# Kernel optimization log

Hardware: AMD Instinct MI355X
Metric: run time of the kernel (lower is better)

The kernel has to match this reference:

```python
import jax, jax.numpy as jnp
import numpy as np

SIZE = 32            # resize target from size=(32,32)
CAL_THRESH = 0.3
WIN = 11             # standard SSIM gaussian window
SIGMA = 1.5
C1 = (0.01 * 255.0) ** 2   # data range 255 (patches are raw pixel values)
C2 = (0.03 * 255.0) ** 2


def _gauss_window():
    g = np.exp(-((np.arange(WIN) - WIN // 2) ** 2) / (2.0 * SIGMA ** 2))
    g = g / g.sum()
    return jnp.asarray(np.outer(g, g), jnp.float32)


def _gconv(x, win):
    # depthwise gaussian blur, same padding; x: [N,C,H,W]
    C = x.shape[1]
    k = jnp.tile(win[None, None], (C, 1, 1, 1))
    return jax.lax.conv_general_dilated(
        x, k, (1, 1), 'SAME',
        dimension_numbers=('NCHW', 'OIHW', 'NCHW'), feature_group_count=C)


def _crop_resize(img, box):
    # img: [C,H,W]; box: [x,y,w,h] with (x,y) = top-left (as used by the crop).
    # Equivalent to img[:, int(y):int(y+h), int(x):int(x+w)] then bilinear
    # F.interpolate to (SIZE,SIZE), align_corners=False (edge-clamped).
    C, H, W = img.shape
    x0 = jnp.floor(box[0]); y0 = jnp.floor(box[1])
    w = jnp.floor(box[0] + box[2]) - x0   # int(x+w) - int(x)
    h = jnp.floor(box[1] + box[3]) - y0
    ys = jnp.clip((jnp.arange(SIZE, dtype=jnp.float32) + 0.5) * (h / SIZE) - 0.5,
                  0.0, jnp.maximum(h - 1.0, 0.0))
    xs = jnp.clip((jnp.arange(SIZE, dtype=jnp.float32) + 0.5) * (w / SIZE) - 0.5,
                  0.0, jnp.maximum(w - 1.0, 0.0))
    yf = jnp.floor(ys); xf = jnp.floor(xs)
    wy = (ys - yf)[None, :, None]   # row weights
    wx = (xs - xf)[None, None, :]   # col weights

    def gi(yi, xi):
        yi = jnp.clip(yi, 0, H - 1).astype(jnp.int32)
        xi = jnp.clip(xi, 0, W - 1).astype(jnp.int32)
        return img[:, yi[:, None], xi[None, :]]  # [C,SIZE,SIZE]

    ylo = yf + y0; yhi = jnp.minimum(yf + 1.0, jnp.maximum(h - 1.0, 0.0)) + y0
    xlo = xf + x0; xhi = jnp.minimum(xf + 1.0, jnp.maximum(w - 1.0, 0.0)) + x0
    top = gi(ylo, xlo) * (1.0 - wx) + gi(ylo, xhi) * wx
    bot = gi(yhi, xlo) * (1.0 - wx) + gi(yhi, xhi) * wx
    return top * (1.0 - wy) + bot * wy


def _pairwise_iou(gt, pr):
    # faithful to get_two_box_iou: (x,y) treated as CENTER here (source quirk)
    g = gt[:, :, None, :]; p = pr[:, None, :, :]
    tl = jnp.maximum(g[..., :2] - g[..., 2:] / 2, p[..., :2] - p[..., 2:] / 2)
    br = jnp.minimum(g[..., :2] + g[..., 2:] / 2, p[..., :2] + p[..., 2:] / 2)
    en = jnp.prod((tl < br).astype(gt.dtype), axis=-1)
    area_i = jnp.prod(br - tl, axis=-1) * en
    area_g = jnp.prod(gt[..., 2:], axis=-1)[:, :, None]
    area_p = jnp.prod(pr[..., 2:], axis=-1)[:, None, :]
    return area_i / (area_g + area_p - area_i + 1e-16)  # [B,G,P]


def setup_inputs() -> dict:
    key = jax.random.key(0)
    k1, k2, k3, k4, k5 = jax.random.split(key, 5)
    B, G, P, H, W = 8, 16, 64, 640, 640
    imgs = jax.random.uniform(k1, (B, 3, H, W), jnp.float32) * 255.0
    xy = jax.random.uniform(k2, (B, G, 2), jnp.float32) * (W - 80.0) + 4.0
    wh = jax.random.uniform(k3, (B, G, 2), jnp.float32) * 56.0 + 8.0
    gt_boxes = jnp.concatenate([xy, wh], axis=-1)
    base = jnp.tile(gt_boxes, (1, P // G, 1))  # preds jittered around GTs so IoU>thresh often
    jit_xy = jax.random.uniform(k4, (B, P, 2), jnp.float32, -4.0, 4.0)
    jit_wh = jax.random.uniform(k5, (B, P, 2), jnp.float32, -4.0, 4.0)
    pred_boxes = jnp.concatenate(
        [base[..., :2] + jit_xy, jnp.maximum(base[..., 2:] + jit_wh, 3.0)], axis=-1)
    return {"gt_boxes": gt_boxes, "pred_boxes": pred_boxes, "imgs": imgs}


def reference(gt_boxes, pred_boxes, imgs):
    B, G = gt_boxes.shape[:2]; P = pred_boxes.shape[1]
    crop = jax.vmap(jax.vmap(_crop_resize, in_axes=(None, 0)), in_axes=(0, 0))
    gt_patch = crop(imgs, gt_boxes)     # [B,G,3,S,S]
    pr_patch = crop(imgs, pred_boxes)   # [B,P,3,S,S]

    iou = _pairwise_iou(gt_boxes, pred_boxes)                    # [B,G,P]
    valid = (pred_boxes[..., 2] > 2) & (pred_boxes[..., 3] > 2)  # [B,P]
    mask = ((iou > CAL_THRESH) & valid[:, None, :]).astype(imgs.dtype)

    # surviving pairs -> dense pair grid (masked mean == mean over survivors)
    x = jnp.broadcast_to(pr_patch[:, None], (B, G, P, 3, SIZE, SIZE)).reshape(-1, 3, SIZE, SIZE)
    y = jnp.broadcast_to(gt_patch[:, :, None], (B, G, P, 3, SIZE, SIZE)).reshape(-1, 3, SIZE, SIZE)

    win = _gauss_window()
    mu1 = _gconv(x, win); mu2 = _gconv(y, win)
    mu1_sq = mu1 * mu1; mu2_sq = mu2 * mu2; mu12 = mu1 * mu2
    s1 = _gconv(x * x, win) - mu1_sq
    s2 = _gconv(y * y, win) - mu2_sq
    s12 = _gconv(x * y, win) - mu12
    ssim_map = ((2 * mu12 + C1) * (2 * s12 + C2)) / ((mu1_sq + mu2_sq + C1) * (s1 + s2 + C2))

    loss = jnp.abs(x / 255.0 - y / 255.0) + (1.0 - ssim_map)    # L1 + SSIM loss, [N,3,S,S]
    loss = loss.reshape(B, G, P, 3, SIZE, SIZE)
    m = mask[:, :, :, None, None, None]
    cnt = jnp.sum(mask) * (3 * SIZE * SIZE)
    total = jnp.sum(loss * m)
    return jnp.where(cnt > 0, total / jnp.maximum(cnt, 1.0), 0.0)
```

## Files before the change

kernel.cpp:

```cpp
#include <hip/hip_runtime.h>
#include <math.h>

#define TSIZE 32
#define WIN 11
#define NB 8
#define NG 16
#define NP 64
#define IMH 640
#define IMW 640
#define NBOX 640
#define NPAIR 8192
#define NCOMP (NPAIR/256)
#define K2GRID 1536

#define C1F 6.5025f
#define C2F 58.5225f

struct GaussW { float g[WIN]; };
struct f4 { float v[4]; };

__global__ __launch_bounds__(256) void gen_patches(
    const float* __restrict__ gt_boxes, const float* __restrict__ pred_boxes,
    const float* __restrict__ imgs,
    float* __restrict__ patches, float* __restrict__ mus, float* __restrict__ gsqs,
    int* __restrict__ pair_list, int* __restrict__ pair_cnt, GaussW gw)
{
    const int bid = blockIdx.x;
    const int tid = threadIdx.x;

    if (bid >= NBOX * 3) {
        const int blk = bid - NBOX * 3;
        const int p = blk * 256 + tid;
        const int b  = p >> 10;
        const int gi = (p >> 6) & 15;
        const int pi = p & 63;
        bool mask;
        {
#pragma clang fp contract(off)
            const float* gb = gt_boxes  + ((size_t)b * NG + gi) * 4;
            const float* pb = pred_boxes + ((size_t)b * NP + pi) * 4;
            const float gx = gb[0], gy = gb[1], gw_ = gb[2], gh = gb[3];
            const float px = pb[0], py = pb[1], pw = pb[2], ph = pb[3];
            const float tlx = fmaxf(gx - gw_ / 2.0f, px - pw / 2.0f);
            const float tly = fmaxf(gy - gh / 2.0f, py - ph / 2.0f);
            const float brx = fminf(gx + gw_ / 2.0f, px + pw / 2.0f);
            const float bry = fminf(gy + gh / 2.0f, py + ph / 2.0f);
            const float en = ((tlx < brx) ? 1.0f : 0.0f) * ((tly < bry) ? 1.0f : 0.0f);
            const float ai = ((brx - tlx) * (bry - tly)) * en;
            const float ag = gw_ * gh;
            const float ap = pw * ph;
            const float iou = ai / (ag + ap - ai + 1e-16f);
            mask = (iou > 0.3f) && (pw > 2.0f) && (ph > 2.0f);
        }
        __shared__ int wcnt[4], woff[4];
        const unsigned long long bal = __ballot(mask);
        const int lane = tid & 63, wid = tid >> 6;
        if (lane == 0) wcnt[wid] = __popcll(bal);
        __syncthreads();
        if (tid == 0) {
            int s = 0;
#pragma unroll
            for (int w = 0; w < 4; ++w) { woff[w] = s; s += wcnt[w]; }
            pair_cnt[blk] = s;
        }
        __syncthreads();
        if (mask) {
            const int pre = __popcll(bal & ((1ull << lane) - 1ull));
            pair_list[blk * 256 + woff[wid] + pre] = p;
        }
        return;
    }

    const int box = bid / 3;
    const int c   = bid - box * 3;
    int b;
    const float* boxp;
    if (box < NB * NG) {
        b = box >> 4;
        boxp = gt_boxes + (size_t)box * 4;
    } else {
        const int q = box - NB * NG;
        b = q >> 6;
        boxp = pred_boxes + (size_t)q * 4;
    }
    const float* __restrict__ ic = imgs + ((size_t)b * 3 + c) * (IMH * IMW);
    float* __restrict__ patch_o = patches + ((size_t)box * 3 + c) * 1024;
    float* __restrict__ mu_o    = mus     + ((size_t)box * 3 + c) * 1024;
    float* __restrict__ gsq_o   = gsqs    + ((size_t)box * 3 + c) * 1024;

    __shared__ int   s_ylo[TSIZE], s_yhi[TSIZE], s_xlo[TSIZE], s_xhi[TSIZE];
    __shared__ float s_wy[TSIZE], s_wx[TSIZE];
    __shared__ __align__(16) float smem[4900];
    float* const sp = smem;
    float* const ta = smem + 1024;
    float* const tb = smem + 2048;

    {
#pragma clang fp contract(off)
        const float b0 = boxp[0], b1 = boxp[1], b2 = boxp[2], b3 = boxp[3];
        const float x0 = floorf(b0), y0 = floorf(b1);
        const float w = floorf(b0 + b2) - x0;
        const float h = floorf(b1 + b3) - y0;

        if (tid < TSIZE) {
            const int t = tid;
            const float hm = fmaxf(h - 1.0f, 0.0f);
            const float scale = h / 32.0f;
            float ys = ((float)t + 0.5f) * scale - 0.5f;
            ys = fminf(fmaxf(ys, 0.0f), hm);
            const float yf = floorf(ys);
            s_wy[t] = ys - yf;
            const float ylo = yf + y0;
            const float yhi = fminf(yf + 1.0f, hm) + y0;
            s_ylo[t] = (int)fminf(fmaxf(ylo, 0.0f), (float)(IMH - 1));
            s_yhi[t] = (int)fminf(fmaxf(yhi, 0.0f), (float)(IMH - 1));
        } else if (tid < 2 * TSIZE) {
            const int t = tid - TSIZE;
            const float wm = fmaxf(w - 1.0f, 0.0f);
            const float scale = w / 32.0f;
            float xs = ((float)t + 0.5f) * scale - 0.5f;
            xs = fminf(fmaxf(xs, 0.0f), wm);
            const float xf = floorf(xs);
            s_wx[t] = xs - xf;
            const float xlo = xf + x0;
            const float xhi = fminf(xf + 1.0f, wm) + x0;
            s_xlo[t] = (int)fminf(fmaxf(xlo, 0.0f), (float)(IMW - 1));
            s_xhi[t] = (int)fminf(fmaxf(xhi, 0.0f), (float)(IMW - 1));
        }
    }
    __syncthreads();

    const int ry0 = s_ylo[0], ry1 = s_yhi[31];
    const int rx0 = s_xlo[0], rx1 = s_xhi[31];
    const int RH = ry1 - ry0 + 1;
    const int RW = rx1 - rx0 + 1;
    const int stride = RW | 1;
    {
        const int wid  = tid >> 6;
        const int lane = tid & 63;
        for (int r = wid; r < RH; r += 4) {
            const float* __restrict__ src = ic + (size_t)(ry0 + r) * IMW + rx0;
            float* __restrict__ dst = smem + r * stride;
            for (int cc = lane; cc < RW; cc += 64) dst[cc] = src[cc];
        }
    }
    __syncthreads();

    const int i  = tid >> 3;
    const int j4 = (tid & 7) << 2;
    const int e4 = (i << 5) + j4;

    float vv[4];
    {
        const int yl = s_ylo[i] - ry0, yh = s_yhi[i] - ry0;
        const float wy = s_wy[i];
#pragma unroll
        for (int q = 0; q < 4; ++q) {
#pragma clang fp contract(off)
            const int j = j4 + q;
            const int xl = s_xlo[j] - rx0, xh = s_xhi[j] - rx0;
            const float wx = s_wx[j];
            const float tl = smem[yl * stride + xl], tr = smem[yl * stride + xh];
            const float bl = smem[yh * stride + xl], br = smem[yh * stride + xh];
            const float top = tl * (1.0f - wx) + tr * wx;
            const float bot = bl * (1.0f - wx) + br * wx;
            vv[q] = top * (1.0f - wy) + bot * wy;
        }
    }
    __syncthreads();

    {
        f4 o; o.v[0] = vv[0]; o.v[1] = vv[1]; o.v[2] = vv[2]; o.v[3] = vv[3];
        *(f4*)&sp[e4] = o;
        *(f4*)&patch_o[e4] = o;
    }
    __syncthreads();

    {
        float pv[14];
#pragma unroll
        for (int k = 0; k < 14; ++k) {
            const int jj = j4 - 5 + k;
            pv[k] = (jj >= 0 && jj < TSIZE) ? sp[(i << 5) + jj] : 0.0f;
        }
        float am[4] = {0.f, 0.f, 0.f, 0.f};
        float aq[4] = {0.f, 0.f, 0.f, 0.f};
#pragma unroll
        for (int k = 0; k < WIN; ++k) {
            const float gk = gw.g[k];
#pragma unroll
            for (int q = 0; q < 4; ++q) {
                const float v = pv[k + q];
                am[q] += gk * v;
                aq[q] += gk * (v * v);
            }
        }
        f4 oa; f4 ob;
#pragma unroll
        for (int q = 0; q < 4; ++q) { oa.v[q] = am[q]; ob.v[q] = aq[q]; }
        *(f4*)&ta[e4] = oa;
        *(f4*)&tb[e4] = ob;
    }
    __syncthreads();

    {
        float cm[4] = {0.f, 0.f, 0.f, 0.f};
        float cq[4] = {0.f, 0.f, 0.f, 0.f};
#pragma unroll
        for (int k = 0; k < WIN; ++k) {
            const int ii = i - 5 + k;
            if (ii >= 0 && ii < TSIZE) {
                const float gk = gw.g[k];
                const f4 m4 = *(const f4*)&ta[(ii << 5) + j4];
                const f4 q4 = *(const f4*)&tb[(ii << 5) + j4];
#pragma unroll
                for (int q = 0; q < 4; ++q) {
                    cm[q] += gk * m4.v[q];
                    cq[q] += gk * q4.v[q];
                }
            }
        }
        f4 om; f4 oq;
#pragma unroll
        for (int q = 0; q < 4; ++q) { om.v[q] = cm[q]; oq.v[q] = cq[q]; }
        *(f4*)&mu_o[e4]  = om;
        *(f4*)&gsq_o[e4] = oq;
    }
}

__global__ __launch_bounds__(256) void pair_kernel(
    const float* __restrict__ patches, const float* __restrict__ mus,
    const float* __restrict__ gsqs,
    const int* __restrict__ pair_list, const int* __restrict__ pair_cnt,
    float* __restrict__ partial, GaussW gw)
{
    __shared__ __align__(16) float sx[1024], sy[1024], tp[1024];
    __shared__ float wred[4];
    __shared__ int cum[NCOMP + 1];
    const int tid = threadIdx.x;

    if (tid == 0) {
        int s = 0;
#pragma unroll
        for (int k = 0; k < NCOMP; ++k) { cum[k] = s; s += pair_cnt[k]; }
        cum[NCOMP] = s;
    }
    __syncthreads();
    const int nw = cum[NCOMP] * 3;

    const int i  = tid >> 3;
    const int j4 = (tid & 7) << 2;
    const int e4 = (i << 5) + j4;

    for (int w = blockIdx.x; w < nw; w += gridDim.x) {
        const int k3 = w / 3;
        const int c  = w - k3 * 3;
        int s = 0;
        while (cum[s + 1] <= k3) ++s;
        const int p  = pair_list[s * 256 + (k3 - cum[s])];
        const int b  = p >> 10;
        const int gi = (p >> 6) & 15;
        const int pi = p & 63;
        const int gbox = b * NG + gi;
        const int pbox = NB * NG + b * NP + pi;
        const size_t po = ((size_t)pbox * 3 + c) * 1024;
        const size_t go = ((size_t)gbox * 3 + c) * 1024;

        const f4 xv = *(const f4*)&patches[po + e4];
        const f4 yv = *(const f4*)&patches[go + e4];
        *(f4*)&sx[e4] = xv;
        *(f4*)&sy[e4] = yv;
        __syncthreads();

        {
            float pv[14];
#pragma unroll
            for (int k = 0; k < 14; ++k) {
                const int jj = j4 - 5 + k;
                pv[k] = (jj >= 0 && jj < TSIZE)
                        ? sx[(i << 5) + jj] * sy[(i << 5) + jj] : 0.0f;
            }
            float a[4] = {0.f, 0.f, 0.f, 0.f};
#pragma unroll
            for (int k = 0; k < WIN; ++k) {
                const float gk = gw.g[k];
#pragma unroll
                for (int q = 0; q < 4; ++q) a[q] += gk * pv[k + q];
            }
            f4 o;
#pragma unroll
            for (int q = 0; q < 4; ++q) o.v[q] = a[q];
            *(f4*)&tp[e4] = o;
        }
        __syncthreads();

        float lsum = 0.0f;
        {
            float cxy[4] = {0.f, 0.f, 0.f, 0.f};
#pragma unroll
            for (int k = 0; k < WIN; ++k) {
                const int ii = i - 5 + k;
                if (ii >= 0 && ii < TSIZE) {
                    const float gk = gw.g[k];
                    const f4 t4 = *(const f4*)&tp[(ii << 5) + j4];
#pragma unroll
                    for (int q = 0; q < 4; ++q) cxy[q] += gk * t4.v[q];
                }
            }
            const f4 mu1 = *(const f4*)&mus[po + e4];
            const f4 mu2 = *(const f4*)&mus[go + e4];
            const f4 q1  = *(const f4*)&gsqs[po + e4];
            const f4 q2  = *(const f4*)&gsqs[go + e4];
#pragma unroll
            for (int q = 0; q < 4; ++q) {
                const float m1 = mu1.v[q], m2 = mu2.v[q];
                const float m1s = m1 * m1, m2s = m2 * m2, m12 = m1 * m2;
                const float s1  = q1.v[q] - m1s;
                const float s2  = q2.v[q] - m2s;
                const float s12 = cxy[q] - m12;
                const float num = (2.0f * m12 + C1F) * (2.0f * s12 + C2F);
                const float den = (m1s + m2s + C1F) * (s1 + s2 + C2F);
                const float ssim = num / den;
                lsum += fabsf(xv.v[q] / 255.0f - yv.v[q] / 255.0f) + (1.0f - ssim);
            }
        }

#pragma unroll
        for (int off = 32; off > 0; off >>= 1) lsum += __shfl_down(lsum, off);
        if ((tid & 63) == 0) wred[tid >> 6] = lsum;
        __syncthreads();
        if (tid == 0) partial[w] = wred[0] + wred[1] + wred[2] + wred[3];
        __syncthreads();
    }
}

__global__ __launch_bounds__(256) void finalize_kernel(
    const int* __restrict__ pair_cnt, const float* __restrict__ partial,
    float* __restrict__ out)
{
    __shared__ float wred[4];
    const int tid = threadIdx.x;
    int n = 0;
#pragma unroll
    for (int k = 0; k < NCOMP; ++k) n += pair_cnt[k];
    const int nw = n * 3;
    float lsum = 0.0f;
    for (int w = tid; w < nw; w += 256) lsum += partial[w];
#pragma unroll
    for (int off = 32; off > 0; off >>= 1) lsum += __shfl_down(lsum, off);
    if ((tid & 63) == 0) wred[tid >> 6] = lsum;
    __syncthreads();
    if (tid == 0) {
        const float total = wred[0] + wred[1] + wred[2] + wred[3];
        out[0] = (n > 0) ? (total / ((float)n * 3072.0f)) : 0.0f;
    }
}

extern "C" void kernel_launch(void* const* d_in, const int* in_sizes, int n_in,
                              void* d_out, int out_size, void* d_ws, size_t ws_size,
                              hipStream_t stream) {
    const float* gt_boxes   = (const float*)d_in[0];
    const float* pred_boxes = (const float*)d_in[1];
    const float* imgs       = (const float*)d_in[2];

    GaussW gw;
    {
        double gd[WIN]; double s = 0.0;
        for (int k = 0; k < WIN; ++k) {
            const double d = (double)(k - WIN / 2);
            gd[k] = exp(-(d * d) / (2.0 * 1.5 * 1.5));
            s += gd[k];
        }
        for (int k = 0; k < WIN; ++k) gw.g[k] = (float)(gd[k] / s);
    }

    float* ws = (float*)d_ws;
    float* patches = ws;
    float* mus     = patches + (size_t)NBOX * 3072;
    float* gsqs    = mus     + (size_t)NBOX * 3072;
    float* partial = gsqs    + (size_t)NBOX * 3072;
    int* pair_list = (int*)(partial + 3 * NPAIR);
    int* pair_cnt  = pair_list + NPAIR;

    gen_patches<<<NBOX * 3 + NCOMP, 256, 0, stream>>>(
        gt_boxes, pred_boxes, imgs, patches, mus, gsqs, pair_list, pair_cnt, gw);

    pair_kernel<<<K2GRID, 256, 0, stream>>>(
        patches, mus, gsqs, pair_list, pair_cnt, partial, gw);

    finalize_kernel<<<1, 256, 0, stream>>>(pair_cnt, partial, (float*)d_out);
}
```

Baseline: 103.9 us.

## Use wavefront shuffles for horizontal blur windows and swizzle LDS tiles

The horizontal pass of the Gaussian blur now reads neighbouring values from adjacent lanes with cross-lane shuffles instead of going through shared memory. This drops the staging arrays and one barrier in both the patch and pair kernels. The intermediate tiles in shared memory use an XOR-like column swizzle to spread the vertical-pass vector loads across banks. The image crop copy is restructured so all row loads are issued before the stores, adding register pressure from the unrolled 17-entry buffer.

```diff
diff --git a/kernel.cpp b/kernel.cpp
--- a/kernel.cpp
+++ b/kernel.cpp
@@ -16,8 +16,40 @@
 #define C1F 6.5025f
 #define C2F 58.5225f
 
+#define SWZ4(row, jq) (((row) << 5) + ((((jq) + (row)) & 7) << 2))
+
 struct GaussW { float g[WIN]; };
 struct f4 { float v[4]; };
+
+__device__ __forceinline__ float shl(float v, int src) {
+    src = src < 0 ? 0 : (src > 63 ? 63 : src);
+    return __shfl(v, src, 64);
+}
+
+__device__ __forceinline__ void row_window(
+    const float* __restrict__ own, int lane, int t, float* __restrict__ pv)
+{
+    const int l = lane;
+    const float a0 = shl(own[0], l - 1), a1 = shl(own[1], l - 1);
+    const float a2 = shl(own[2], l - 1), a3 = shl(own[3], l - 1);
+    const float b0 = shl(own[0], l + 1), b1 = shl(own[1], l + 1);
+    const float b2 = shl(own[2], l + 1), b3 = shl(own[3], l + 1);
+    const float m3 = shl(own[3], l - 2);
+    const float p0 = shl(own[0], l + 2);
+    const bool vm1 = (t >= 1), vm2 = (t >= 2);
+    const bool vp1 = (t <= 6), vp2 = (t <= 5);
+    pv[0]  = vm2 ? m3 : 0.0f;
+    pv[1]  = vm1 ? a0 : 0.0f;
+    pv[2]  = vm1 ? a1 : 0.0f;
+    pv[3]  = vm1 ? a2 : 0.0f;
+    pv[4]  = vm1 ? a3 : 0.0f;
+    pv[5]  = own[0]; pv[6] = own[1]; pv[7] = own[2]; pv[8] = own[3];
+    pv[9]  = vp1 ? b0 : 0.0f;
+    pv[10] = vp1 ? b1 : 0.0f;
+    pv[11] = vp1 ? b2 : 0.0f;
+    pv[12] = vp1 ? b3 : 0.0f;
+    pv[13] = vp2 ? p0 : 0.0f;
+}
 
 __global__ __launch_bounds__(256) void gen_patches(
     const float* __restrict__ gt_boxes, const float* __restrict__ pred_boxes,
@@ -90,10 +122,9 @@
 
     __shared__ int   s_ylo[TSIZE], s_yhi[TSIZE], s_xlo[TSIZE], s_xhi[TSIZE];
     __shared__ float s_wy[TSIZE], s_wx[TSIZE];
-    __shared__ __align__(16) float smem[4900];
-    float* const sp = smem;
-    float* const ta = smem + 1024;
-    float* const tb = smem + 2048;
+    __shared__ __align__(16) float smem[4704];
+    float* const ta = smem;
+    float* const tb = smem + 1024;
 
     {
 #pragma clang fp contract(off)
@@ -135,19 +166,33 @@
     const int RH = ry1 - ry0 + 1;
     const int RW = rx1 - rx0 + 1;
     const int stride = RW | 1;
-    {
-        const int wid  = tid >> 6;
-        const int lane = tid & 63;
-        for (int r = wid; r < RH; r += 4) {
-            const float* __restrict__ src = ic + (size_t)(ry0 + r) * IMW + rx0;
-            float* __restrict__ dst = smem + r * stride;
-            for (int cc = lane; cc < RW; cc += 64) dst[cc] = src[cc];
+    const int wv = tid >> 6, lane = tid & 63;
+    {
+        float rbuf[17];
+        const bool cl = lane < RW;
+#pragma unroll
+        for (int u = 0; u < 17; ++u) {
+            const int r = wv + (u << 2);
+            rbuf[u] = (r < RH && cl)
+                      ? ic[(size_t)(ry0 + r) * IMW + rx0 + lane] : 0.0f;
+        }
+        const bool c2 = (64 + lane) < RW;
+#pragma unroll
+        for (int u = 0; u < 17; ++u) {
+            const int r = wv + (u << 2);
+            if (r < RH) {
+                if (cl) smem[r * stride + lane] = rbuf[u];
+                if (c2) smem[r * stride + 64 + lane] =
+                            ic[(size_t)(ry0 + r) * IMW + rx0 + 64 + lane];
+            }
         }
     }
     __syncthreads();
 
     const int i  = tid >> 3;
-    const int j4 = (tid & 7) << 2;
+    const int t  = tid & 7;
+    const int j4 = t << 2;
+    const int jq = t;
     const int e4 = (i << 5) + j4;
 
     float vv[4];
@@ -171,20 +216,13 @@
 
     {
         f4 o; o.v[0] = vv[0]; o.v[1] = vv[1]; o.v[2] = vv[2]; o.v[3] = vv[3];
-        *(f4*)&sp[e4] = o;
         *(f4*)&patch_o[e4] = o;
     }
-    __syncthreads();
 
     {
         float pv[14];
-#pragma unroll
-        for (int k = 0; k < 14; ++k) {
-            const int jj = j4 - 5 + k;
-            pv[k] = (jj >= 0 && jj < TSIZE) ? sp[(i << 5) + jj] : 0.0f;
-        }
-        float am[4] = {0.f, 0.f, 0.f, 0.f};
-        float aq[4] = {0.f, 0.f, 0.f, 0.f};
+        row_window(vv, lane, t, pv);
+        float am[4] = {0.f,0.f,0.f,0.f}, aq[4] = {0.f,0.f,0.f,0.f};
 #pragma unroll
         for (int k = 0; k < WIN; ++k) {
             const float gk = gw.g[k];
@@ -195,32 +233,31 @@
                 aq[q] += gk * (v * v);
             }
         }
-        f4 oa; f4 ob;
+        f4 oa, ob;
 #pragma unroll
         for (int q = 0; q < 4; ++q) { oa.v[q] = am[q]; ob.v[q] = aq[q]; }
-        *(f4*)&ta[e4] = oa;
-        *(f4*)&tb[e4] = ob;
-    }
-    __syncthreads();
-
-    {
-        float cm[4] = {0.f, 0.f, 0.f, 0.f};
-        float cq[4] = {0.f, 0.f, 0.f, 0.f};
+        *(f4*)&ta[SWZ4(i, jq)] = oa;
+        *(f4*)&tb[SWZ4(i, jq)] = ob;
+    }
+    __syncthreads();
+
+    {
+        float cm[4] = {0.f,0.f,0.f,0.f}, cq[4] = {0.f,0.f,0.f,0.f};
 #pragma unroll
         for (int k = 0; k < WIN; ++k) {
             const int ii = i - 5 + k;
             if (ii >= 0 && ii < TSIZE) {
                 const float gk = gw.g[k];
-                const f4 m4 = *(const f4*)&ta[(ii << 5) + j4];
-                const f4 q4 = *(const f4*)&tb[(ii << 5) + j4];
+                const f4 m4 = *(const f4*)&ta[SWZ4(ii, jq)];
+                const f4 s4 = *(const f4*)&tb[SWZ4(ii, jq)];
 #pragma unroll
                 for (int q = 0; q < 4; ++q) {
                     cm[q] += gk * m4.v[q];
-                    cq[q] += gk * q4.v[q];
+                    cq[q] += gk * s4.v[q];
                 }
             }
         }
-        f4 om; f4 oq;
+        f4 om, oq;
 #pragma unroll
         for (int q = 0; q < 4; ++q) { om.v[q] = cm[q]; oq.v[q] = cq[q]; }
         *(f4*)&mu_o[e4]  = om;
@@ -234,7 +271,7 @@
     const int* __restrict__ pair_list, const int* __restrict__ pair_cnt,
     float* __restrict__ partial, GaussW gw)
 {
-    __shared__ __align__(16) float sx[1024], sy[1024], tp[1024];
+    __shared__ __align__(16) float tp[1024];
     __shared__ float wred[4];
     __shared__ int cum[NCOMP + 1];
     const int tid = threadIdx.x;
@@ -249,8 +286,11 @@
     const int nw = cum[NCOMP] * 3;
 
     const int i  = tid >> 3;
-    const int j4 = (tid & 7) << 2;
+    const int t  = tid & 7;
+    const int j4 = t << 2;
+    const int jq = t;
     const int e4 = (i << 5) + j4;
+    const int lane = tid & 63;
 
     for (int w = blockIdx.x; w < nw; w += gridDim.x) {
         const int k3 = w / 3;
@@ -268,19 +308,14 @@
 
         const f4 xv = *(const f4*)&patches[po + e4];
         const f4 yv = *(const f4*)&patches[go + e4];
-        *(f4*)&sx[e4] = xv;
-        *(f4*)&sy[e4] = yv;
-        __syncthreads();
 
         {
+            float prod[4];
+#pragma unroll
+            for (int q = 0; q < 4; ++q) prod[q] = xv.v[q] * yv.v[q];
             float pv[14];
-#pragma unroll
-            for (int k = 0; k < 14; ++k) {
-                const int jj = j4 - 5 + k;
-                pv[k] = (jj >= 0 && jj < TSIZE)
-                        ? sx[(i << 5) + jj] * sy[(i << 5) + jj] : 0.0f;
-            }
-            float a[4] = {0.f, 0.f, 0.f, 0.f};
+            row_window(prod, lane, t, pv);
+            float a[4] = {0.f,0.f,0.f,0.f};
 #pragma unroll
             for (int k = 0; k < WIN; ++k) {
                 const float gk = gw.g[k];
@@ -290,19 +325,19 @@
             f4 o;
 #pragma unroll
             for (int q = 0; q < 4; ++q) o.v[q] = a[q];
-            *(f4*)&tp[e4] = o;
+            *(f4*)&tp[SWZ4(i, jq)] = o;
         }
         __syncthreads();
 
         float lsum = 0.0f;
         {
-            float cxy[4] = {0.f, 0.f, 0.f, 0.f};
+            float cxy[4] = {0.f,0.f,0.f,0.f};
 #pragma unroll
             for (int k = 0; k < WIN; ++k) {
                 const int ii = i - 5 + k;
                 if (ii >= 0 && ii < TSIZE) {
                     const float gk = gw.g[k];
-                    const f4 t4 = *(const f4*)&tp[(ii << 5) + j4];
+                    const f4 t4 = *(const f4*)&tp[SWZ4(ii, jq)];
 #pragma unroll
                     for (int q = 0; q < 4; ++q) cxy[q] += gk * t4.v[q];
                 }
@@ -327,7 +362,7 @@
 
 #pragma unroll
         for (int off = 32; off > 0; off >>= 1) lsum += __shfl_down(lsum, off);
-        if ((tid & 63) == 0) wred[tid >> 6] = lsum;
+        if (lane == 0) wred[tid >> 6] = lsum;
         __syncthreads();
         if (tid == 0) partial[w] = wred[0] + wred[1] + wred[2] + wred[3];
         __syncthreads();
```

Result: faster. 101.0 us (-2.8%).
